# Kernel tuning notes

Hardware: AMD Instinct MI355X
Metric: run time of the kernel (lower is better)

The kernel has to match this reference:

```python
import jax, jax.numpy as jnp
import numpy as np

EPS = 1e-8
BINS = 32


def setup_inputs() -> dict:
    key = jax.random.key(0)
    k0, k1, k2 = jax.random.split(key, 3)
    B, L, D = 1, 320, 128
    residx = jnp.arange(B * L, dtype=jnp.int32).reshape(B, L)
    mask = jnp.ones((B, L), dtype=bool)
    emb_table = jax.random.normal(k0, (2 * BINS + 2, D), dtype=jnp.float32) * 0.02
    pair_feats = jax.random.normal(k1, (B, L, L, D), dtype=jnp.float32)
    predxyz = jax.random.normal(k2, (B, 3, L, L), dtype=jnp.float32)
    # maskdiag zeros the diagonal (self-displacement), as used for predxyz * maskdiag
    maskdiag = (1.0 - jnp.eye(L, dtype=jnp.float32))[None, None, :, :]
    return {
        "residx": residx,
        "mask": mask,
        "emb_table": emb_table,
        "pair_feats": pair_feats,
        "predxyz": predxyz,
        "maskdiag": maskdiag,
    }


def relative_position(residx, mask, emb_table):
    # diff in [-BINS, BINS] -> indices in [1, 2*BINS+1]; masked pairs -> index 0
    diff = residx[:, None, :] - residx[:, :, None]          # [B, L, L]
    diff = jnp.clip(diff, -BINS, BINS) + (BINS + 1)
    pair_mask = mask[:, None, :] & mask[:, :, None]
    diff = jnp.where(pair_mask, diff, 0)
    return emb_table[diff]                                   # [B, L, L, D]


def get_cadist_avg(pxyz):
    # pxyz: [B, 3, L, L]; relative displacement over the last two residue axes
    rel = pxyz[:, :, :, None, :] - pxyz[:, :, :, :, None]    # [B, 3, L, L, L]
    dist = jnp.sqrt(jnp.sum(rel * rel, axis=1) + EPS)        # [B, L, L, L]
    return jnp.mean(dist, axis=1)                            # [B, L, L]


def reference(residx, mask, emb_table, pair_feats, predxyz, maskdiag):
    # pairwise positional embedding added to the pair state (trunk input)
    z = pair_feats + relative_position(residx, mask, emb_table)  # [B, L, L, D]
    # geometry head: masked coordinates -> residual distance average
    pxyz = predxyz * maskdiag                                    # [B, 3, L, L]
    cadistavg = get_cadist_avg(pxyz)                             # [B, L, L]
    return (z, pxyz, cadistavg)
```

## Files before the change

kernel.cpp:

```cpp
#include <hip/hip_runtime.h>

#define L 320
#define PLANE (L * L)
#define Z_ELEMS (L * L * 128)
#define PX_ELEMS (3 * PLANE)
#define CAD_ELEMS PLANE

#define NCADB 400
#define NPXB  75
#define NZB   1600

typedef float nfloat4 __attribute__((ext_vector_type(4)));

__device__ __forceinline__ void nt_store4(float4* p, float x, float y, float z, float w)
{
    nfloat4 v = {x, y, z, w};
    __builtin_nontemporal_store(v, (nfloat4*)p);
}

__global__ __launch_bounds__(256) void fused_kernel(
    const int*    __restrict__ residx,
    const float4* __restrict__ emb4,
    const float4* __restrict__ pf4,
    const float*  __restrict__ pred,
    const float4* __restrict__ md4,
    float4*       __restrict__ z4,
    float4*       __restrict__ px4,
    float*        __restrict__ cad)
{
    const int b = blockIdx.x;
    const int t = threadIdx.x;

    if (b < NCADB) {
        __shared__ float sj[3][16][36];
        __shared__ float sk[3][16][36];

        const int j0 = (b / 20) * 16;
        const int k0 = (b % 20) * 16;
        const int jj = t >> 4;
        const int kk = t & 15;

        const int  s_ii  = t >> 3;
        const int  s_seg = t & 7;
        const bool s_isk = s_seg >= 4;
        const int  s_s4  = (s_seg & 3) * 4;
        const int  s_col = (s_isk ? k0 : j0) + s_s4;
        const float4* pred4 = (const float4*)pred;

        float4 stage[3];
        #pragma unroll
        for (int c = 0; c < 3; ++c)
            stage[c] = pred4[c * 25600 + s_ii * 80 + (s_col >> 2)];

        float acc = 0.0f;

        for (int ch = 0; ch < 10; ++ch) {
            const int i_row = ch * 32 + s_ii;
            float* dstb = s_isk ? &sk[0][0][0] : &sj[0][0][0];
            #pragma unroll
            for (int c = 0; c < 3; ++c) {
                const float4 v = stage[c];
                #pragma unroll
                for (int s = 0; s < 4; ++s) {
                    float val = (s == 0) ? v.x : (s == 1) ? v.y : (s == 2) ? v.z : v.w;
                    if (i_row == s_col + s) val = 0.0f;
                    dstb[(c * 16 + s_s4 + s) * 36 + s_ii] = val;
                }
            }
            __syncthreads();

            if (ch < 9) {
                #pragma unroll
                for (int c = 0; c < 3; ++c)
                    stage[c] = pred4[c * 25600 + ((ch + 1) * 32 + s_ii) * 80 + (s_col >> 2)];
            }

            #pragma unroll
            for (int g = 0; g < 8; ++g) {
                const float4 xj = *(const float4*)&sj[0][jj][g * 4];
                const float4 yj = *(const float4*)&sj[1][jj][g * 4];
                const float4 zj = *(const float4*)&sj[2][jj][g * 4];
                const float4 xk = *(const float4*)&sk[0][kk][g * 4];
                const float4 yk = *(const float4*)&sk[1][kk][g * 4];
                const float4 zk = *(const float4*)&sk[2][kk][g * 4];
                #pragma unroll
                for (int w = 0; w < 4; ++w) {
                    const float dx = ((w==0)?xk.x:(w==1)?xk.y:(w==2)?xk.z:xk.w)
                                   - ((w==0)?xj.x:(w==1)?xj.y:(w==2)?xj.z:xj.w);
                    const float dy = ((w==0)?yk.x:(w==1)?yk.y:(w==2)?yk.z:yk.w)
                                   - ((w==0)?yj.x:(w==1)?yj.y:(w==2)?yj.z:yj.w);
                    const float dz = ((w==0)?zk.x:(w==1)?zk.y:(w==2)?zk.z:zk.w)
                                   - ((w==0)?zj.x:(w==1)?zj.y:(w==2)?zj.z:zj.w);
                    acc += sqrtf(fmaf(dx, dx, fmaf(dy, dy, fmaf(dz, dz, 1e-8f))));
                }
            }
            __syncthreads();
        }

        cad[(j0 + jj) * L + (k0 + kk)] = acc * (1.0f / L);

    } else if (b < NCADB + NPXB) {
        const int pb = b - NCADB;
        const float4* pred4 = (const float4*)pred;
        #pragma unroll
        for (int it = 0; it < 4; ++it) {
            const int n = pb * 1024 + it * 256 + t;
            int m = n;
            if      (m >= 2 * (PLANE / 4)) m -= 2 * (PLANE / 4);
            else if (m >=     (PLANE / 4)) m -=     (PLANE / 4);
            const float4 a  = pred4[n];
            const float4 mm = md4[m];
            nt_store4(&px4[n],
                      a.x * mm.x, a.y * mm.y, a.z * mm.z, a.w * mm.w);
        }

    } else {
        const int zb    = b - NCADB - NPXB;
        const int i     = zb / 5;
        const int chunk = zb % 5;
        const int ri    = residx[i];

        #pragma unroll
        for (int it = 0; it < 8; ++it) {
            const int off = chunk * 2048 + it * 256 + t;
            const int j   = off >> 5;
            const int d4  = off & 31;
            int diff = residx[j] - ri;
            diff = min(max(diff, -32), 32) + 33;
            const float4 a = pf4[i * 10240 + off];
            const float4 e = emb4[diff * 32 + d4];
            nt_store4(&z4[i * 10240 + off],
                      a.x + e.x, a.y + e.y, a.z + e.z, a.w + e.w);
        }
    }
}

extern "C" void kernel_launch(void* const* d_in, const int* in_sizes, int n_in,
                              void* d_out, int out_size, void* d_ws, size_t ws_size,
                              hipStream_t stream)
{
    const int*   residx = (const int*)  d_in[0];
    const float* emb    = (const float*)d_in[2];
    const float* pf     = (const float*)d_in[3];
    const float* pred   = (const float*)d_in[4];
    const float* md     = (const float*)d_in[5];

    float* z   = (float*)d_out;
    float* px  = z  + Z_ELEMS;
    float* cad = px + PX_ELEMS;

    fused_kernel<<<NCADB + NPXB + NZB, 256, 0, stream>>>(
        residx, (const float4*)emb, (const float4*)pf, pred, (const float4*)md,
        (float4*)z, (float4*)px, cad);
}
```

Baseline: 128.9 us.

## Exploit cadist symmetry, swizzle shared-memory layout, and use regular stores for z

Since the distance is symmetric in (j,k), only upper-triangular 16x16 tiles are computed (210 blocks instead of 400), and off-diagonal tiles write both the result and its transpose. The shared-memory index is XOR-swizzled on both the store and the float4 read side to reduce LDS bank conflicts. The z output now uses ordinary stores instead of nontemporal ones. The transposed cad write is uncoalesced, and the tile-index decode uses a small serial loop.

```diff
diff --git a/kernel.cpp b/kernel.cpp
--- a/kernel.cpp
+++ b/kernel.cpp
@@ -6,7 +6,7 @@
 #define PX_ELEMS (3 * PLANE)
 #define CAD_ELEMS PLANE
 
-#define NCADB 400
+#define NCADB 210
 #define NPXB  75
 #define NZB   1600
 
@@ -17,6 +17,8 @@
     nfloat4 v = {x, y, z, w};
     __builtin_nontemporal_store(v, (nfloat4*)p);
 }
+
+#define SWZ(col) (((col) & 12) << 1)
 
 __global__ __launch_bounds__(256) void fused_kernel(
     const int*    __restrict__ residx,
@@ -35,8 +37,12 @@
         __shared__ float sj[3][16][36];
         __shared__ float sk[3][16][36];
 
-        const int j0 = (b / 20) * 16;
-        const int k0 = (b % 20) * 16;
+        int tj = 0, rem = b;
+        while (rem >= 20 - tj) { rem -= 20 - tj; ++tj; }
+        const int tk = tj + rem;
+        const int j0 = tj * 16;
+        const int k0 = tk * 16;
+
         const int jj = t >> 4;
         const int kk = t & 15;
 
@@ -45,6 +51,7 @@
         const bool s_isk = s_seg >= 4;
         const int  s_s4  = (s_seg & 3) * 4;
         const int  s_col = (s_isk ? k0 : j0) + s_s4;
+        const int  s_swz = SWZ(s_s4);
         const float4* pred4 = (const float4*)pred;
 
         float4 stage[3];
@@ -64,7 +71,7 @@
                 for (int s = 0; s < 4; ++s) {
                     float val = (s == 0) ? v.x : (s == 1) ? v.y : (s == 2) ? v.z : v.w;
                     if (i_row == s_col + s) val = 0.0f;
-                    dstb[(c * 16 + s_s4 + s) * 36 + s_ii] = val;
+                    dstb[(c * 16 + s_s4 + s) * 36 + (s_ii ^ s_swz)] = val;
                 }
             }
             __syncthreads();
@@ -75,14 +82,16 @@
                     stage[c] = pred4[c * 25600 + ((ch + 1) * 32 + s_ii) * 80 + (s_col >> 2)];
             }
 
+            const int jswz = SWZ(jj);
+            const int kswz = SWZ(kk);
             #pragma unroll
             for (int g = 0; g < 8; ++g) {
-                const float4 xj = *(const float4*)&sj[0][jj][g * 4];
-                const float4 yj = *(const float4*)&sj[1][jj][g * 4];
-                const float4 zj = *(const float4*)&sj[2][jj][g * 4];
-                const float4 xk = *(const float4*)&sk[0][kk][g * 4];
-                const float4 yk = *(const float4*)&sk[1][kk][g * 4];
-                const float4 zk = *(const float4*)&sk[2][kk][g * 4];
+                const float4 xj = *(const float4*)&sj[0][jj][(g * 4) ^ jswz];
+                const float4 yj = *(const float4*)&sj[1][jj][(g * 4) ^ jswz];
+                const float4 zj = *(const float4*)&sj[2][jj][(g * 4) ^ jswz];
+                const float4 xk = *(const float4*)&sk[0][kk][(g * 4) ^ kswz];
+                const float4 yk = *(const float4*)&sk[1][kk][(g * 4) ^ kswz];
+                const float4 zk = *(const float4*)&sk[2][kk][(g * 4) ^ kswz];
                 #pragma unroll
                 for (int w = 0; w < 4; ++w) {
                     const float dx = ((w==0)?xk.x:(w==1)?xk.y:(w==2)?xk.z:xk.w)
@@ -97,7 +106,10 @@
             __syncthreads();
         }
 
-        cad[(j0 + jj) * L + (k0 + kk)] = acc * (1.0f / L);
+        const float v = acc * (1.0f / L);
+        cad[(j0 + jj) * L + (k0 + kk)] = v;
+        if (tj != tk)
+            cad[(k0 + kk) * L + (j0 + jj)] = v;
 
     } else if (b < NCADB + NPXB) {
         const int pb = b - NCADB;
@@ -129,8 +141,8 @@
             diff = min(max(diff, -32), 32) + 33;
             const float4 a = pf4[i * 10240 + off];
             const float4 e = emb4[diff * 32 + d4];
-            nt_store4(&z4[i * 10240 + off],
-                      a.x + e.x, a.y + e.y, a.z + e.z, a.w + e.w);
+            z4[i * 10240 + off] =
+                make_float4(a.x + e.x, a.y + e.y, a.z + e.z, a.w + e.w);
         }
     }
 }
```

Measured after the change: 120.4 us. -6.6%, faster.

## Exploit cadist symmetry with upper-triangle 32x32 tiles, split-i atomics, swizzled LDS

Applied to the files above, without the earlier changes.

The cadist part now computes only upper-triangular 32x32 (j,k) tiles, because distance is symmetric. Each block handles 64 of the 320 i rows, and partial sums are accumulated into both (j,k) and (k,j) with atomicAdd after a memset of the output. Each thread now computes a 2x2 micro-tile from XOR-swizzled shared memory to improve register reuse and avoid bank conflicts. The z store also switches from nontemporal to a normal store. The trade is an extra memset launch, atomic traffic, and float sums that are no longer deterministic.

```diff
diff --git a/kernel.cpp b/kernel.cpp
--- a/kernel.cpp
+++ b/kernel.cpp
@@ -6,7 +6,9 @@
 #define PX_ELEMS (3 * PLANE)
 #define CAD_ELEMS PLANE
 
-#define NCADB 400
+#define NTILES 55
+#define ISPLIT 5
+#define NCADB (NTILES * ISPLIT)
 #define NPXB  75
 #define NZB   1600
 
@@ -17,6 +19,8 @@
     nfloat4 v = {x, y, z, w};
     __builtin_nontemporal_store(v, (nfloat4*)p);
 }
+
+#define FQ(q) (((q) & 6) << 2)
 
 __global__ __launch_bounds__(256) void fused_kernel(
     const int*    __restrict__ residx,
@@ -32,72 +36,116 @@
     const int t = threadIdx.x;
 
     if (b < NCADB) {
-        __shared__ float sj[3][16][36];
-        __shared__ float sk[3][16][36];
-
-        const int j0 = (b / 20) * 16;
-        const int k0 = (b % 20) * 16;
-        const int jj = t >> 4;
-        const int kk = t & 15;
-
-        const int  s_ii  = t >> 3;
-        const int  s_seg = t & 7;
-        const bool s_isk = s_seg >= 4;
-        const int  s_s4  = (s_seg & 3) * 4;
-        const int  s_col = (s_isk ? k0 : j0) + s_s4;
+        __shared__ float sj[3][32][36];
+        __shared__ float sk[3][32][36];
+
+        const int spl = b / NTILES;
+        const int tb  = b - spl * NTILES;
+        int tj = 0, rem = tb;
+        while (rem >= 10 - tj) { rem -= 10 - tj; ++tj; }
+        const int tk = tj + rem;
+        const int j0 = tj * 32, k0 = tk * 32;
+
+        const int jj  = t >> 4;
+        const int kk  = t & 15;
+        const int sii = t >> 3;
+        const int q   = t & 7;
+        const int Fs  = FQ(q);
+        const int ist = spl * 64;
+
         const float4* pred4 = (const float4*)pred;
 
-        float4 stage[3];
-        #pragma unroll
-        for (int c = 0; c < 3; ++c)
-            stage[c] = pred4[c * 25600 + s_ii * 80 + (s_col >> 2)];
-
-        float acc = 0.0f;
-
-        for (int ch = 0; ch < 10; ++ch) {
-            const int i_row = ch * 32 + s_ii;
-            float* dstb = s_isk ? &sk[0][0][0] : &sj[0][0][0];
+        float4 stg[3][2];
+        #pragma unroll
+        for (int c = 0; c < 3; ++c) {
+            stg[c][0] = pred4[c * 25600 + (ist + sii) * 80 + (j0 >> 2) + q];
+            stg[c][1] = pred4[c * 25600 + (ist + sii) * 80 + (k0 >> 2) + q];
+        }
+
+        float a00 = 0.f, a01 = 0.f, a10 = 0.f, a11 = 0.f;
+
+        #pragma unroll
+        for (int ch = 0; ch < 2; ++ch) {
+            const int irow = ist + ch * 32 + sii;
             #pragma unroll
             for (int c = 0; c < 3; ++c) {
-                const float4 v = stage[c];
+                const float4 vj = stg[c][0];
+                const float4 vk = stg[c][1];
                 #pragma unroll
                 for (int s = 0; s < 4; ++s) {
-                    float val = (s == 0) ? v.x : (s == 1) ? v.y : (s == 2) ? v.z : v.w;
-                    if (i_row == s_col + s) val = 0.0f;
-                    dstb[(c * 16 + s_s4 + s) * 36 + s_ii] = val;
+                    const int cl = q * 4 + s;
+                    float fj = (s == 0) ? vj.x : (s == 1) ? vj.y : (s == 2) ? vj.z : vj.w;
+                    float fk = (s == 0) ? vk.x : (s == 1) ? vk.y : (s == 2) ? vk.z : vk.w;
+                    if (irow == j0 + cl) fj = 0.0f;
+                    if (irow == k0 + cl) fk = 0.0f;
+                    sj[c][cl][sii ^ Fs] = fj;
+                    sk[c][cl][sii ^ Fs] = fk;
                 }
             }
             __syncthreads();
 
-            if (ch < 9) {
-                #pragma unroll
-                for (int c = 0; c < 3; ++c)
-                    stage[c] = pred4[c * 25600 + ((ch + 1) * 32 + s_ii) * 80 + (s_col >> 2)];
+            if (ch == 0) {
+                #pragma unroll
+                for (int c = 0; c < 3; ++c) {
+                    stg[c][0] = pred4[c * 25600 + (ist + 32 + sii) * 80 + (j0 >> 2) + q];
+                    stg[c][1] = pred4[c * 25600 + (ist + 32 + sii) * 80 + (k0 >> 2) + q];
+                }
             }
+
+            const int FjA = FQ(jj >> 2),        FjB = FQ((jj + 16) >> 2);
+            const int FkA = FQ(kk >> 2),        FkB = FQ((kk + 16) >> 2);
 
             #pragma unroll
             for (int g = 0; g < 8; ++g) {
-                const float4 xj = *(const float4*)&sj[0][jj][g * 4];
-                const float4 yj = *(const float4*)&sj[1][jj][g * 4];
-                const float4 zj = *(const float4*)&sj[2][jj][g * 4];
-                const float4 xk = *(const float4*)&sk[0][kk][g * 4];
-                const float4 yk = *(const float4*)&sk[1][kk][g * 4];
-                const float4 zk = *(const float4*)&sk[2][kk][g * 4];
+                const int g4 = g * 4;
+                float4 jA[3], jB[3], kA[3], kB[3];
+                #pragma unroll
+                for (int c = 0; c < 3; ++c) {
+                    jA[c] = *(const float4*)&sj[c][jj     ][g4 ^ FjA];
+                    jB[c] = *(const float4*)&sj[c][jj + 16][g4 ^ FjB];
+                    kA[c] = *(const float4*)&sk[c][kk     ][g4 ^ FkA];
+                    kB[c] = *(const float4*)&sk[c][kk + 16][g4 ^ FkB];
+                }
                 #pragma unroll
                 for (int w = 0; w < 4; ++w) {
-                    const float dx = ((w==0)?xk.x:(w==1)?xk.y:(w==2)?xk.z:xk.w)
-                                   - ((w==0)?xj.x:(w==1)?xj.y:(w==2)?xj.z:xj.w);
-                    const float dy = ((w==0)?yk.x:(w==1)?yk.y:(w==2)?yk.z:yk.w)
-                                   - ((w==0)?yj.x:(w==1)?yj.y:(w==2)?yj.z:yj.w);
-                    const float dz = ((w==0)?zk.x:(w==1)?zk.y:(w==2)?zk.z:zk.w)
-                                   - ((w==0)?zj.x:(w==1)?zj.y:(w==2)?zj.z:zj.w);
-                    acc += sqrtf(fmaf(dx, dx, fmaf(dy, dy, fmaf(dz, dz, 1e-8f))));
+                    const float jAx = (w==0)?jA[0].x:(w==1)?jA[0].y:(w==2)?jA[0].z:jA[0].w;
+                    const float jAy = (w==0)?jA[1].x:(w==1)?jA[1].y:(w==2)?jA[1].z:jA[1].w;
+                    const float jAz = (w==0)?jA[2].x:(w==1)?jA[2].y:(w==2)?jA[2].z:jA[2].w;
+                    const float jBx = (w==0)?jB[0].x:(w==1)?jB[0].y:(w==2)?jB[0].z:jB[0].w;
+                    const float jBy = (w==0)?jB[1].x:(w==1)?jB[1].y:(w==2)?jB[1].z:jB[1].w;
+                    const float jBz = (w==0)?jB[2].x:(w==1)?jB[2].y:(w==2)?jB[2].z:jB[2].w;
+                    const float kAx = (w==0)?kA[0].x:(w==1)?kA[0].y:(w==2)?kA[0].z:kA[0].w;
+                    const float kAy = (w==0)?kA[1].x:(w==1)?kA[1].y:(w==2)?kA[1].z:kA[1].w;
+                    const float kAz = (w==0)?kA[2].x:(w==1)?kA[2].y:(w==2)?kA[2].z:kA[2].w;
+                    const float kBx = (w==0)?kB[0].x:(w==1)?kB[0].y:(w==2)?kB[0].z:kB[0].w;
+                    const float kBy = (w==0)?kB[1].x:(w==1)?kB[1].y:(w==2)?kB[1].z:kB[1].w;
+                    const float kBz = (w==0)?kB[2].x:(w==1)?kB[2].y:(w==2)?kB[2].z:kB[2].w;
+
+                    float dx = kAx - jAx, dy = kAy - jAy, dz = kAz - jAz;
+                    a00 += sqrtf(fmaf(dx, dx, fmaf(dy, dy, fmaf(dz, dz, 1e-8f))));
+                    dx = kBx - jAx; dy = kBy - jAy; dz = kBz - jAz;
+                    a01 += sqrtf(fmaf(dx, dx, fmaf(dy, dy, fmaf(dz, dz, 1e-8f))));
+                    dx = kAx - jBx; dy = kAy - jBy; dz = kAz - jBz;
+                    a10 += sqrtf(fmaf(dx, dx, fmaf(dy, dy, fmaf(dz, dz, 1e-8f))));
+                    dx = kBx - jBx; dy = kBy - jBy; dz = kBz - jBz;
+                    a11 += sqrtf(fmaf(dx, dx, fmaf(dy, dy, fmaf(dz, dz, 1e-8f))));
                 }
             }
             __syncthreads();
         }
 
-        cad[(j0 + jj) * L + (k0 + kk)] = acc * (1.0f / L);
+        const float s00 = a00 * (1.0f / L), s01 = a01 * (1.0f / L);
+        const float s10 = a10 * (1.0f / L), s11 = a11 * (1.0f / L);
+        atomicAdd(&cad[(j0 + jj     ) * L + (k0 + kk     )], s00);
+        atomicAdd(&cad[(j0 + jj     ) * L + (k0 + kk + 16)], s01);
+        atomicAdd(&cad[(j0 + jj + 16) * L + (k0 + kk     )], s10);
+        atomicAdd(&cad[(j0 + jj + 16) * L + (k0 + kk + 16)], s11);
+        if (tj != tk) {
+            atomicAdd(&cad[(k0 + kk     ) * L + (j0 + jj     )], s00);
+            atomicAdd(&cad[(k0 + kk + 16) * L + (j0 + jj     )], s01);
+            atomicAdd(&cad[(k0 + kk     ) * L + (j0 + jj + 16)], s10);
+            atomicAdd(&cad[(k0 + kk + 16) * L + (j0 + jj + 16)], s11);
+        }
 
     } else if (b < NCADB + NPXB) {
         const int pb = b - NCADB;
@@ -129,8 +177,8 @@
             diff = min(max(diff, -32), 32) + 33;
             const float4 a = pf4[i * 10240 + off];
             const float4 e = emb4[diff * 32 + d4];
-            nt_store4(&z4[i * 10240 + off],
-                      a.x + e.x, a.y + e.y, a.z + e.z, a.w + e.w);
+            z4[i * 10240 + off] =
+                make_float4(a.x + e.x, a.y + e.y, a.z + e.z, a.w + e.w);
         }
     }
 }
@@ -149,6 +197,8 @@
     float* px  = z  + Z_ELEMS;
     float* cad = px + PX_ELEMS;
 
+    hipMemsetAsync(cad, 0, CAD_ELEMS * sizeof(float), stream);
+
     fused_kernel<<<NCADB + NPXB + NZB, 256, 0, stream>>>(
         residx, (const float4*)emb, (const float4*)pf, pred, (const float4*)md,
         (float4*)z, (float4*)px, cad);
```

Result: faster. 121.4 us (-5.8%).
